# Kernel tuning notes

Hardware: AMD Instinct MI355X
Metric: run time of the kernel (lower is better)

The kernel has to match this reference:

```python
import jax, jax.numpy as jnp
import numpy as np


def _topk_masked_softmax(attn, k):
    # Keep only the top-k entries per row (last dim), softmax over them.
    _, idx = jax.lax.top_k(attn, k)  # [b, nh, C, k]
    mask = jnp.put_along_axis(
        jnp.zeros(attn.shape, dtype=bool), idx, True, axis=-1, inplace=False
    )
    return jax.nn.softmax(jnp.where(mask, attn, -jnp.inf), axis=-1)


def setup_inputs() -> dict:
    key = jax.random.key(0)
    k0, k1, k2, k3, k4 = jax.random.split(key, 5)
    b, nh, C = 8, 8, 512
    attn = jax.random.normal(k0, (b, nh, C, C), dtype=jnp.float32)
    # In the torch module these are Parameters initialized to 0.2; use random
    # positive scalars of similar scale for a non-degenerate baseline.
    w1 = jax.random.uniform(k1, (1,), dtype=jnp.float32)
    w2 = jax.random.uniform(k2, (1,), dtype=jnp.float32)
    w3 = jax.random.uniform(k3, (1,), dtype=jnp.float32)
    w4 = jax.random.uniform(k4, (1,), dtype=jnp.float32)
    return {"attn": attn, "w1": w1, "w2": w2, "w3": w3, "w4": w4}


def reference(attn, w1, w2, w3, w4):
    C = attn.shape[-1]
    a1 = _topk_masked_softmax(attn, int(C / 2))
    a2 = _topk_masked_softmax(attn, int(C * 2 / 3))
    a3 = _topk_masked_softmax(attn, int(C * 3 / 4))
    a4 = _topk_masked_softmax(attn, int(C * 4 / 5))
    return a1 * w1 + a2 * w2 + a3 * w3 + a4 * w4
```

## Files before the change

kernel.cpp:

```cpp
#include <hip/hip_runtime.h>
#include <math.h>

#define ROW_C 512
#define NBIN 2048
#define NPACK (NBIN / 2)

__global__ __launch_bounds__(256) void topk_ms_kernel(
    const float* __restrict__ attn,
    const float* __restrict__ w1p, const float* __restrict__ w2p,
    const float* __restrict__ w3p, const float* __restrict__ w4p,
    float* __restrict__ out)
{
    __shared__ __align__(16) unsigned hist_all[4][NPACK];

    const int lane = threadIdx.x & 63;
    const int wv   = threadIdx.x >> 6;
    unsigned* h = hist_all[wv];
    int4* hv = (int4*)h;

    const long long row  = (long long)blockIdx.x * 4 + wv;
    const long long base = row * ROW_C + lane * 8;

    const float4 A = *reinterpret_cast<const float4*>(attn + base);
    const float4 B = *reinterpret_cast<const float4*>(attn + base + 4);
    float orig[8] = {A.x, A.y, A.z, A.w, B.x, B.y, B.z, B.w};

    unsigned key[8];
    int bin[8];
    #pragma unroll
    for (int s = 0; s < 8; ++s) {
        const unsigned u = __float_as_uint(orig[s]);
        key[s] = (u & 0x80000000u) ? ~u : (u | 0x80000000u);
        const float y = fminf(fmaxf(orig[s], -7.9f), 7.9f) + 24.0f;
        bin[s] = (int)((__float_as_uint(y) >> 12) & 0x7FFu);
    }

    {
        const int4 z = make_int4(0, 0, 0, 0);
        hv[lane] = z; hv[lane + 64] = z; hv[lane + 128] = z; hv[lane + 192] = z;
    }

    #pragma unroll
    for (int s = 0; s < 8; ++s) {
        const int j  = bin[s] >> 1;
        const int ph = j ^ (((j >> 5) & 7) << 2);
        atomicAdd(&h[ph], (bin[s] & 1) ? 0x10000u : 1u);
    }

    unsigned pp[16];
    #pragma unroll
    for (int k = 0; k < 4; ++k) {
        const int b  = 4 * lane + k;
        const int pb = b ^ ((b >> 3) & 7);
        const int4 v = hv[pb];
        pp[4 * k]     = (unsigned)v.x;
        pp[4 * k + 1] = (unsigned)v.y;
        pp[4 * k + 2] = (unsigned)v.z;
        pp[4 * k + 3] = (unsigned)v.w;
    }
    unsigned run = 0;
    #pragma unroll
    for (int j = 0; j < 16; ++j) {
        const unsigned q = pp[j] + (pp[j] << 16);
        pp[j] = q + run * 0x10001u;
        run = pp[j] >> 16;
    }
    unsigned incl = run;
    #pragma unroll
    for (int off = 1; off < 64; off <<= 1) {
        const unsigned t = __shfl_up(incl, off, 64);
        if (lane >= off) incl += t;
    }
    const unsigned bmul = (incl - run) * 0x10001u;
    #pragma unroll
    for (int j = 0; j < 16; ++j) pp[j] += bmul;
    #pragma unroll
    for (int k = 0; k < 4; ++k) {
        const int b  = 4 * lane + k;
        const int pb = b ^ ((b >> 3) & 7);
        hv[pb] = make_int4((int)pp[4 * k], (int)pp[4 * k + 1],
                           (int)pp[4 * k + 2], (int)pp[4 * k + 3]);
    }

    int bsel = 0, Rwithin = 0;
    if (lane < 4) {
        const int KS[4] = {256, 341, 384, 409};
        const int K = KS[lane];
        const int T = 512 - K + 1;
        int lo = -1, hi = NBIN - 1;
        unsigned pbv = 512u;
        #pragma unroll
        for (int it = 0; it < 11; ++it) {
            const int mid = (lo + hi) >> 1;
            const int jm  = mid >> 1;
            const int ph  = jm ^ (((jm >> 5) & 7) << 2);
            const unsigned w  = h[ph];
            const unsigned pv = (mid & 1) ? (w >> 16) : (w & 0xFFFFu);
            const bool ge = ((int)pv >= T);
            hi  = ge ? mid : hi;
            pbv = ge ? pv  : pbv;
            lo  = ge ? lo  : mid;
        }
        bsel    = hi;
        Rwithin = K - 512 + (int)pbv;
    }

    int b_r[4], R_r[4];
    #pragma unroll
    for (int r = 0; r < 4; ++r) {
        b_r[r] = __shfl(bsel, r, 64);
        R_r[r] = __shfl(Rwithin, r, 64);
    }

    unsigned tk[4]; int need[4], cnteq[4];
    #pragma unroll
    for (int r = 0; r < 4; ++r) {
        unsigned cm[8];
        #pragma unroll
        for (int s = 0; s < 8; ++s)
            cm[s] = (bin[s] == b_r[r]) ? key[s] : 0u;
        int R = R_r[r];
        unsigned t; int c;
        while (true) {
            unsigned mk = cm[0];
            #pragma unroll
            for (int s = 1; s < 8; ++s) mk = (cm[s] > mk) ? cm[s] : mk;
            #pragma unroll
            for (int off = 32; off >= 1; off >>= 1) {
                const unsigned o = __shfl_xor(mk, off, 64);
                mk = (o > mk) ? o : mk;
            }
            t = mk;
            c = 0;
            #pragma unroll
            for (int s = 0; s < 8; ++s)
                c += (int)__popcll(__ballot(cm[s] == t));
            if (c >= R) break;
            R -= c;
            #pragma unroll
            for (int s = 0; s < 8; ++s)
                if (cm[s] == t) cm[s] = 0u;
        }
        tk[r] = t; need[r] = R; cnteq[r] = c;
    }

    int fl[8] = {0, 0, 0, 0, 0, 0, 0, 0};
    #pragma unroll
    for (int r = 0; r < 4; ++r) {
        const unsigned t = tk[r];
        if (need[r] == cnteq[r]) {
            #pragma unroll
            for (int s = 0; s < 8; ++s)
                fl[s] |= ((int)(key[s] >= t)) << r;
        } else {
            const unsigned long long ltm = (1ull << lane) - 1ull;
            int basec = 0;
            #pragma unroll
            for (int s = 0; s < 8; ++s)
                basec += (int)__popcll(__ballot(key[s] == t) & ltm);
            int own = 0;
            #pragma unroll
            for (int s = 0; s < 8; ++s) {
                const bool eq = (key[s] == t);
                if (key[s] > t || (eq && (basec + own) < need[r]))
                    fl[s] |= (1 << r);
                own += eq ? 1 : 0;
            }
        }
    }

    float eo[8];
    #pragma unroll
    for (int s = 0; s < 8; ++s) eo[s] = __expf(orig[s]);

    float z0 = 0.f, z1 = 0.f, z2 = 0.f, z3 = 0.f;
    #pragma unroll
    for (int s = 0; s < 8; ++s) {
        z0 += (fl[s] & 1) ? eo[s] : 0.f;
        z1 += (fl[s] & 2) ? eo[s] : 0.f;
        z2 += (fl[s] & 4) ? eo[s] : 0.f;
        z3 += (fl[s] & 8) ? eo[s] : 0.f;
    }
    #pragma unroll
    for (int off = 32; off >= 1; off >>= 1) {
        z0 += __shfl_xor(z0, off, 64);
        z1 += __shfl_xor(z1, off, 64);
        z2 += __shfl_xor(z2, off, 64);
        z3 += __shfl_xor(z3, off, 64);
    }

    const float wz0 = w1p[0] / z0;
    const float wz1 = w2p[0] / z1;
    const float wz2 = w3p[0] / z2;
    const float wz3 = w4p[0] / z3;

    float res[8];
    #pragma unroll
    for (int s = 0; s < 8; ++s) {
        float c = 0.f;
        c += (fl[s] & 1) ? wz0 : 0.f;
        c += (fl[s] & 2) ? wz1 : 0.f;
        c += (fl[s] & 4) ? wz2 : 0.f;
        c += (fl[s] & 8) ? wz3 : 0.f;
        res[s] = eo[s] * c;
    }
    *reinterpret_cast<float4*>(out + base)     = make_float4(res[0], res[1], res[2], res[3]);
    *reinterpret_cast<float4*>(out + base + 4) = make_float4(res[4], res[5], res[6], res[7]);
}

extern "C" void kernel_launch(void* const* d_in, const int* in_sizes, int n_in,
                              void* d_out, int out_size, void* d_ws, size_t ws_size,
                              hipStream_t stream) {
    const float* attn = (const float*)d_in[0];
    const float* w1   = (const float*)d_in[1];
    const float* w2   = (const float*)d_in[2];
    const float* w3   = (const float*)d_in[3];
    const float* w4   = (const float*)d_in[4];
    float* out = (float*)d_out;

    int rows = in_sizes[0] / ROW_C;
    int blocks = (rows + 3) / 4;
    topk_ms_kernel<<<blocks, 256, 0, stream>>>(attn, w1, w2, w3, w4, out);
}
```

Measured before the change: 148.4 us.

## Replace histogram scan and binary search with ballot-based bin selection

Drops the full per-bin prefix-sum write-back to shared memory. Each lane now sums its 32 bins, a wave-wide scan plus ballots finds the lane holding the threshold bin for each of the four k values, and a short local scan picks the exact bin. A new shortcut skips the iterative tie-resolution loop when the selected bin is taken whole. The histogram range is also narrowed to [-3.9, 3.9] for finer bins, exp is hoisted earlier, and division is replaced by a fast reciprocal, which may slightly change rounding.

New measurement: 136.4 us. 1.09x faster.

```diff
diff --git a/kernel.cpp b/kernel.cpp
--- a/kernel.cpp
+++ b/kernel.cpp
@@ -23,16 +23,18 @@
 
     const float4 A = *reinterpret_cast<const float4*>(attn + base);
     const float4 B = *reinterpret_cast<const float4*>(attn + base + 4);
-    float orig[8] = {A.x, A.y, A.z, A.w, B.x, B.y, B.z, B.w};
+    const float orig[8] = {A.x, A.y, A.z, A.w, B.x, B.y, B.z, B.w};
 
     unsigned key[8];
     int bin[8];
+    float eo[8];
     #pragma unroll
     for (int s = 0; s < 8; ++s) {
         const unsigned u = __float_as_uint(orig[s]);
         key[s] = (u & 0x80000000u) ? ~u : (u | 0x80000000u);
-        const float y = fminf(fmaxf(orig[s], -7.9f), 7.9f) + 24.0f;
+        const float y = fminf(fmaxf(orig[s], -3.90625f), 3.90625f) + 12.0f;
         bin[s] = (int)((__float_as_uint(y) >> 12) & 0x7FFu);
+        eo[s] = __expf(orig[s]);
     }
 
     {
@@ -43,116 +45,135 @@
     #pragma unroll
     for (int s = 0; s < 8; ++s) {
         const int j  = bin[s] >> 1;
-        const int ph = j ^ (((j >> 5) & 7) << 2);
+        const int ph = j ^ ((j >> 3) & 0x1C);
         atomicAdd(&h[ph], (bin[s] & 1) ? 0x10000u : 1u);
     }
 
-    unsigned pp[16];
+    unsigned ps = 0;
     #pragma unroll
     for (int k = 0; k < 4; ++k) {
         const int b  = 4 * lane + k;
         const int pb = b ^ ((b >> 3) & 7);
         const int4 v = hv[pb];
-        pp[4 * k]     = (unsigned)v.x;
-        pp[4 * k + 1] = (unsigned)v.y;
-        pp[4 * k + 2] = (unsigned)v.z;
-        pp[4 * k + 3] = (unsigned)v.w;
-    }
-    unsigned run = 0;
-    #pragma unroll
-    for (int j = 0; j < 16; ++j) {
-        const unsigned q = pp[j] + (pp[j] << 16);
-        pp[j] = q + run * 0x10001u;
-        run = pp[j] >> 16;
-    }
-    unsigned incl = run;
+        ps += (unsigned)v.x + (unsigned)v.y + (unsigned)v.z + (unsigned)v.w;
+    }
+    const unsigned tot = (ps & 0xFFFFu) + (ps >> 16);
+
+    unsigned incl = tot;
     #pragma unroll
     for (int off = 1; off < 64; off <<= 1) {
         const unsigned t = __shfl_up(incl, off, 64);
         if (lane >= off) incl += t;
     }
-    const unsigned bmul = (incl - run) * 0x10001u;
-    #pragma unroll
-    for (int j = 0; j < 16; ++j) pp[j] += bmul;
-    #pragma unroll
-    for (int k = 0; k < 4; ++k) {
-        const int b  = 4 * lane + k;
-        const int pb = b ^ ((b >> 3) & 7);
-        hv[pb] = make_int4((int)pp[4 * k], (int)pp[4 * k + 1],
-                           (int)pp[4 * k + 2], (int)pp[4 * k + 3]);
-    }
-
-    int bsel = 0, Rwithin = 0;
+    const unsigned excl = incl - tot;
+
+    const unsigned long long Ba = __ballot(incl >= 257u);
+    const unsigned long long Bb = __ballot(incl >= 172u);
+    const unsigned long long Bc = __ballot(incl >= 129u);
+    const unsigned long long Bd = __ballot(incl >= 104u);
+    const int l0 = __ffsll(Ba) - 1, l1 = __ffsll(Bb) - 1,
+              l2 = __ffsll(Bc) - 1, l3 = __ffsll(Bd) - 1;
+
+    const int lsel = (lane == 0) ? l0 : (lane == 1) ? l1 : (lane == 2) ? l2 : l3;
+    const int Tr   = (lane == 0) ? 257 : (lane == 1) ? 172 : (lane == 2) ? 129 : 104;
+    const int Kr   = (lane == 0) ? 256 : (lane == 1) ? 341 : (lane == 2) ? 384 : 409;
+    const unsigned exl = __shfl(excl, lsel & 63, 64);
+
+    unsigned brR = 0u;
     if (lane < 4) {
-        const int KS[4] = {256, 341, 384, 409};
-        const int K = KS[lane];
-        const int T = 512 - K + 1;
-        int lo = -1, hi = NBIN - 1;
-        unsigned pbv = 512u;
+        const int Tl = Tr - (int)exl;
+        const unsigned T16 = (unsigned)Tl << 16;
+        const int jbase = lsel << 4;
+        const int xr = ((lsel >> 1) & 7) << 2;
+        unsigned w[16];
         #pragma unroll
-        for (int it = 0; it < 11; ++it) {
-            const int mid = (lo + hi) >> 1;
-            const int jm  = mid >> 1;
-            const int ph  = jm ^ (((jm >> 5) & 7) << 2);
-            const unsigned w  = h[ph];
-            const unsigned pv = (mid & 1) ? (w >> 16) : (w & 0xFFFFu);
-            const bool ge = ((int)pv >= T);
-            hi  = ge ? mid : hi;
-            pbv = ge ? pv  : pbv;
-            lo  = ge ? lo  : mid;
-        }
-        bsel    = hi;
-        Rwithin = K - 512 + (int)pbv;
-    }
-
-    int b_r[4], R_r[4];
+        for (int q = 0; q < 4; ++q) {
+            const int pw = ((jbase + (q << 2)) ^ xr) >> 2;
+            const int4 v = hv[pw];
+            w[4*q+0] = (unsigned)v.x; w[4*q+1] = (unsigned)v.y;
+            w[4*q+2] = (unsigned)v.z; w[4*q+3] = (unsigned)v.w;
+        }
+        unsigned run = 0, pcap = 0, rcap = 0; int jcap = 0; bool found = false;
+        #pragma unroll
+        for (int j = 0; j < 16; ++j) {
+            const unsigned p = (w[j] + (w[j] << 16)) + (run + (run << 16));
+            const bool ge   = (p >= T16);
+            const bool take = ge && !found;
+            pcap = take ? p   : pcap;
+            rcap = take ? run : rcap;
+            jcap = take ? j   : jcap;
+            found = found || ge;
+            run = p >> 16;
+        }
+        const int  lo   = (int)(pcap & 0xFFFFu);
+        const bool ev   = (lo >= Tl);
+        const int  bsel = (lsel << 5) + (jcap << 1) + (ev ? 0 : 1);
+        const int  locp = ev ? lo : (int)(pcap >> 16);
+        const int  prvp = ev ? (int)rcap : lo;
+        const int  R    = Kr - 512 + (int)exl + locp;
+        const unsigned allin = (prvp == Tl - 1) ? 1u : 0u;
+        brR = ((unsigned)bsel << 17) | (allin << 16) | (unsigned)R;
+    }
+
+    int br_[4], Rr_[4], al_[4];
     #pragma unroll
     for (int r = 0; r < 4; ++r) {
-        b_r[r] = __shfl(bsel, r, 64);
-        R_r[r] = __shfl(Rwithin, r, 64);
+        const unsigned v = __shfl(brR, r, 64);
+        br_[r] = (int)(v >> 17);
+        al_[r] = (int)((v >> 16) & 1u);
+        Rr_[r] = (int)(v & 0xFFFFu);
     }
 
     unsigned tk[4]; int need[4], cnteq[4];
     #pragma unroll
     for (int r = 0; r < 4; ++r) {
-        unsigned cm[8];
-        #pragma unroll
-        for (int s = 0; s < 8; ++s)
-            cm[s] = (bin[s] == b_r[r]) ? key[s] : 0u;
-        int R = R_r[r];
-        unsigned t; int c;
-        while (true) {
-            unsigned mk = cm[0];
-            #pragma unroll
-            for (int s = 1; s < 8; ++s) mk = (cm[s] > mk) ? cm[s] : mk;
-            #pragma unroll
-            for (int off = 32; off >= 1; off >>= 1) {
-                const unsigned o = __shfl_xor(mk, off, 64);
-                mk = (o > mk) ? o : mk;
+        tk[r] = 0u; need[r] = 0; cnteq[r] = 0;
+        if (!al_[r]) {
+            unsigned cm[8];
+            #pragma unroll
+            for (int s = 0; s < 8; ++s)
+                cm[s] = (bin[s] == br_[r]) ? key[s] : 0u;
+            int R = Rr_[r];
+            unsigned t; int c;
+            while (true) {
+                unsigned mk = cm[0];
+                #pragma unroll
+                for (int s = 1; s < 8; ++s) mk = (cm[s] > mk) ? cm[s] : mk;
+                #pragma unroll
+                for (int off = 32; off >= 1; off >>= 1) {
+                    const unsigned o = __shfl_xor(mk, off, 64);
+                    mk = (o > mk) ? o : mk;
+                }
+                t = mk;
+                c = 0;
+                #pragma unroll
+                for (int s = 0; s < 8; ++s)
+                    c += (int)__popcll(__ballot(cm[s] == t));
+                if (c >= R) break;
+                R -= c;
+                #pragma unroll
+                for (int s = 0; s < 8; ++s)
+                    if (cm[s] == t) cm[s] = 0u;
             }
-            t = mk;
-            c = 0;
-            #pragma unroll
-            for (int s = 0; s < 8; ++s)
-                c += (int)__popcll(__ballot(cm[s] == t));
-            if (c >= R) break;
-            R -= c;
-            #pragma unroll
-            for (int s = 0; s < 8; ++s)
-                if (cm[s] == t) cm[s] = 0u;
-        }
-        tk[r] = t; need[r] = R; cnteq[r] = c;
+            tk[r] = t; need[r] = R; cnteq[r] = c;
+        }
     }
 
     int fl[8] = {0, 0, 0, 0, 0, 0, 0, 0};
     #pragma unroll
     for (int r = 0; r < 4; ++r) {
-        const unsigned t = tk[r];
-        if (need[r] == cnteq[r]) {
+        if (al_[r]) {
+            const int bb = br_[r];
+            #pragma unroll
+            for (int s = 0; s < 8; ++s)
+                fl[s] |= ((int)(bin[s] >= bb)) << r;
+        } else if (need[r] == cnteq[r]) {
+            const unsigned t = tk[r];
             #pragma unroll
             for (int s = 0; s < 8; ++s)
                 fl[s] |= ((int)(key[s] >= t)) << r;
         } else {
+            const unsigned t = tk[r];
             const unsigned long long ltm = (1ull << lane) - 1ull;
             int basec = 0;
             #pragma unroll
@@ -169,10 +190,6 @@
         }
     }
 
-    float eo[8];
-    #pragma unroll
-    for (int s = 0; s < 8; ++s) eo[s] = __expf(orig[s]);
-
     float z0 = 0.f, z1 = 0.f, z2 = 0.f, z3 = 0.f;
     #pragma unroll
     for (int s = 0; s < 8; ++s) {
@@ -189,10 +206,10 @@
         z3 += __shfl_xor(z3, off, 64);
     }
 
-    const float wz0 = w1p[0] / z0;
-    const float wz1 = w2p[0] / z1;
-    const float wz2 = w3p[0] / z2;
-    const float wz3 = w4p[0] / z3;
+    const float wz0 = w1p[0] * __builtin_amdgcn_rcpf(z0);
+    const float wz1 = w2p[0] * __builtin_amdgcn_rcpf(z1);
+    const float wz2 = w3p[0] * __builtin_amdgcn_rcpf(z2);
+    const float wz3 = w4p[0] * __builtin_amdgcn_rcpf(z3);
 
     float res[8];
     #pragma unroll
```
